# Kernel optimization log

Hardware: AMD Instinct MI355X
Metric: run time of the kernel (lower is better)

Reference implementation:

```python
import jax, jax.numpy as jnp
import numpy as np

N, D, E = 40000, 128, 640000
SLOPE = 0.01  # torch LeakyReLU default negative_slope

def leaky(x):
    return jnp.where(x >= 0, x, SLOPE * x)

def setup_inputs() -> dict:
    key = jax.random.key(0)
    ks = jax.random.split(key, 12)
    s = lambda fan_in: 1.0 / np.sqrt(fan_in)
    inp = {
        "x": jax.random.normal(ks[0], (N, D), jnp.float32),
        "pos": jax.random.normal(ks[1], (N, 3), jnp.float32),
        "edge_index": jax.random.randint(ks[2], (2, E), 0, N, jnp.int64),
        # mlp_h: Linear(D,D) -> LeakyReLU -> Linear(D,3) -> Tanh
        "Wh1": jax.random.uniform(ks[3], (D, D), jnp.float32, -s(D), s(D)),
        "bh1": jnp.zeros((D,), jnp.float32),
        "Wh2": jax.random.uniform(ks[4], (D, 3), jnp.float32, -s(D), s(D)),
        "bh2": jnp.zeros((3,), jnp.float32),
        # mlp_f: Linear(D+3, D) -> LeakyReLU
        "Wf1": jax.random.uniform(ks[5], (D + 3, D), jnp.float32, -s(D + 3), s(D + 3)),
        "bf1": jnp.zeros((D,), jnp.float32),
        # mlp_g: Linear(D,D) -> LeakyReLU -> Linear(D,D)
        "Wg1": jax.random.uniform(ks[6], (D, D), jnp.float32, -s(D), s(D)),
        "bg1": jnp.zeros((D,), jnp.float32),
        "Wg2": jax.random.uniform(ks[7], (D, D), jnp.float32, -s(D), s(D)),
        "bg2": jnp.zeros((D,), jnp.float32),
    }
    return inp

def reference(x, pos, edge_index, Wh1, bh1, Wh2, bh2, Wf1, bf1, Wg1, bg1, Wg2, bg2):
    src = edge_index[0]  # j (source / neighbor)
    dst = edge_index[1]  # i (target / center)
    n = x.shape[0]
    # mlp_h per node: predicted position offset delta_i
    delta = jnp.tanh(leaky(x @ Wh1 + bh1) @ Wh2 + bh2)  # [N, 3]
    # per-edge message: mlp_f(cat(pos_j - pos_i + delta_i, x_j))
    rel = pos[src] - pos[dst] + delta[dst]               # [E, 3]
    e = jnp.concatenate([rel, x[src]], axis=-1)          # [E, D+3]
    msg = leaky(e @ Wf1 + bf1)                           # [E, D]
    # sum aggregation to target nodes
    aggr = jax.ops.segment_sum(msg, dst, num_segments=n) # [N, D]
    # node update with residual
    out = x + (leaky(aggr @ Wg1 + bg1) @ Wg2 + bg2)      # [N, D]
    return out
```

## Files before the change

### kernel.cpp

```cpp
#include <hip/hip_runtime.h>

#define NN 40000
#define DD 128
#define EE 640000
#define SLOPE 0.01f
#define CAP 64

typedef __attribute__((ext_vector_type(8))) short  short8;
typedef __attribute__((ext_vector_type(8))) unsigned short ushort8;
typedef __attribute__((ext_vector_type(4))) float  floatx4;

__device__ __forceinline__ float leaky1(float v) { return v >= 0.f ? v : v * SLOPE; }

__device__ __forceinline__ unsigned short f2bf(float f) {
    unsigned int u = __float_as_uint(f);
    u += 0x7fffu + ((u >> 16) & 1u);
    return (unsigned short)(u >> 16);
}

__global__ __launch_bounds__(256) void k_init(
    const float* __restrict__ Wh1, const float* __restrict__ Wf1,
    const float* __restrict__ Wg1, const float* __restrict__ Wg2,
    int* __restrict__ cnt, unsigned short* __restrict__ pk)
{
    const int gid = blockIdx.x * 256 + threadIdx.x;
    if (gid < NN) cnt[gid] = 0;

    if (gid < 8192) {
        const int mat = gid >> 11;
        const int rem = gid & 2047;
        const int ct  = rem >> 8;
        const int kc  = (rem >> 6) & 3;
        const int l   = rem & 63;
        const float* W = (mat == 0) ? Wh1 : (mat == 1) ? (Wf1 + 3 * DD)
                       : (mat == 2) ? Wg1 : Wg2;
        const int n  = ct * 16 + (l & 15);
        const int k0 = kc * 32 + (l >> 4) * 8;
        ushort8 v;
        #pragma unroll
        for (int j = 0; j < 8; ++j) v[j] = f2bf(W[(size_t)(k0 + j) * DD + n]);
        *(ushort8*)(pk + (size_t)gid * 8) = v;
    }
}

__global__ __launch_bounds__(256) void k_node_pre(
    const float* __restrict__ x,
    const unsigned short* __restrict__ pk,
    const float* __restrict__ pos, const float* __restrict__ Wf1,
    const float* __restrict__ bh1, const float* __restrict__ Wh2,
    const float* __restrict__ bh2, const float* __restrict__ bf1,
    unsigned short* __restrict__ ub, float* __restrict__ delta)
{
    __shared__ unsigned short ul[64 * 136];
    const int t  = threadIdx.x;
    const int w  = t >> 6, l = t & 63;
    const int lm = l & 15, q = l >> 4;
    const bool upath = blockIdx.x < 625;
    const int tile = upath ? blockIdx.x : blockIdx.x - 625;
    const int rowb = tile * 64;
    const int row0 = rowb + w * 16;

    const unsigned short* pkm = upath ? (pk + 16384) : pk;

    floatx4 acc[8];
    #pragma unroll
    for (int ct = 0; ct < 8; ++ct) acc[ct] = 0.f;

    #pragma unroll
    for (int kc = 0; kc < 4; ++kc) {
        const float* xp = x + (size_t)(row0 + lm) * DD + kc * 32 + q * 8;
        const float4 v0 = *(const float4*)(xp);
        const float4 v1 = *(const float4*)(xp + 4);
        ushort8 au;
        au[0] = f2bf(v0.x); au[1] = f2bf(v0.y); au[2] = f2bf(v0.z); au[3] = f2bf(v0.w);
        au[4] = f2bf(v1.x); au[5] = f2bf(v1.y); au[6] = f2bf(v1.z); au[7] = f2bf(v1.w);
        const short8 a = *(short8*)&au;
        #pragma unroll
        for (int ct = 0; ct < 8; ++ct) {
            const short8 b = *(const short8*)(pkm + (size_t)((ct * 4 + kc) * 64 + l) * 8);
            acc[ct] = __builtin_amdgcn_mfma_f32_16x16x32_bf16(a, b, acc[ct], 0, 0, 0);
        }
    }

    if (upath) {
        float px[4][3];
        #pragma unroll
        for (int r = 0; r < 4; ++r) {
            const int rr = row0 + q * 4 + r;
            px[r][0] = pos[rr * 3 + 0];
            px[r][1] = pos[rr * 3 + 1];
            px[r][2] = pos[rr * 3 + 2];
        }
        #pragma unroll
        for (int ct = 0; ct < 8; ++ct) {
            const int col = ct * 16 + lm;
            const float bfv = bf1[col];
            const float w0 = Wf1[0 * DD + col];
            const float w1 = Wf1[1 * DD + col];
            const float w2 = Wf1[2 * DD + col];
            #pragma unroll
            for (int r = 0; r < 4; ++r) {
                const float uv = acc[ct][r] + bfv
                               + px[r][0] * w0 + px[r][1] * w1 + px[r][2] * w2;
                ul[(w * 16 + q * 4 + r) * 136 + col] = f2bf(uv);
            }
        }
        __syncthreads();
        #pragma unroll
        for (int k = 0; k < 4; ++k) {
            const int idx = t + k * 256;
            const int row = idx >> 4;
            const int c8  = (idx & 15) * 8;
            *(ushort8*)(ub + (size_t)(rowb + row) * DD + c8) =
                *(const ushort8*)(ul + row * 136 + c8);
        }
    } else {
        float p[4][3] = {};
        #pragma unroll
        for (int ct = 0; ct < 8; ++ct) {
            const int col = ct * 16 + lm;
            const float b1 = bh1[col];
            const float wh20 = Wh2[col * 3 + 0];
            const float wh21 = Wh2[col * 3 + 1];
            const float wh22 = Wh2[col * 3 + 2];
            #pragma unroll
            for (int r = 0; r < 4; ++r) {
                const float hv = leaky1(acc[ct][r] + b1);
                p[r][0] += hv * wh20;
                p[r][1] += hv * wh21;
                p[r][2] += hv * wh22;
            }
        }
        #pragma unroll
        for (int m = 1; m < 16; m <<= 1) {
            #pragma unroll
            for (int r = 0; r < 4; ++r) {
                #pragma unroll
                for (int k = 0; k < 3; ++k)
                    p[r][k] += __shfl_xor(p[r][k], m);
            }
        }
        if (lm < 12) {
            const int r = lm / 3, k = lm - 3 * (lm / 3);
            delta[(size_t)(row0 + q * 4 + r) * 3 + k] = tanhf(p[r][k] + bh2[k]);
        }
    }
}

__global__ __launch_bounds__(256) void k_scatter(const int* __restrict__ ei,
                                                 int* __restrict__ cnt,
                                                 int* __restrict__ esrc)
{
    const int g   = blockIdx.x & 7;
    const int lb  = blockIdx.x >> 3;
    const int dlo = g * 5000;
    const int dhi = dlo + 5000;

    for (int e = lb * 256 + threadIdx.x; e < EE; e += 65536) {
        const int dst = ei[EE + e];
        if (dst >= dlo && dst < dhi) {
            const int src = ei[e];
            const int p = atomicAdd(&cnt[dst], 1);
            if (p < CAP) esrc[(size_t)dst * CAP + p] = src;
        }
    }
}

__global__ __launch_bounds__(256) void k_gather(
    const int* __restrict__ cnt, const int* __restrict__ esrc,
    const float* __restrict__ pos, const float* __restrict__ delta,
    const float* __restrict__ Wf1, const unsigned short* __restrict__ ub,
    unsigned short* __restrict__ aggrb)
{
    const int t    = threadIdx.x;
    const int lane = t & 63;
    const int n    = blockIdx.x * 4 + (t >> 6);
    const int c2   = lane * 2;

    const float2 w0 = *(const float2*)(Wf1 + 0 * DD + c2);
    const float2 w1 = *(const float2*)(Wf1 + 1 * DD + c2);
    const float2 w2 = *(const float2*)(Wf1 + 2 * DD + c2);

    const float q0 = delta[n * 3 + 0] - pos[n * 3 + 0];
    const float q1 = delta[n * 3 + 1] - pos[n * 3 + 1];
    const float q2 = delta[n * 3 + 2] - pos[n * 3 + 2];

    const float v0 = q0 * w0.x + q1 * w1.x + q2 * w2.x;
    const float v1 = q0 * w0.y + q1 * w1.y + q2 * w2.y;

    const int s_all = esrc[(size_t)n * CAP + lane];
    const int d = min(cnt[n], CAP);

    float a0 = 0.f, a1 = 0.f, b0 = 0.f, b1 = 0.f;

    for (int j = 0; j < d; j += 8) {
        unsigned int u[8];
        bool vld[8];
        #pragma unroll
        for (int k = 0; k < 8; ++k) {
            const int jj = j + k;
            vld[k] = jj < d;
            int src = __shfl(s_all, jj & 63);
            src = vld[k] ? src : 0;
            u[k] = *(const unsigned int*)(ub + (size_t)src * DD + c2);
        }
        #pragma unroll
        for (int k = 0; k < 8; ++k) {
            const float e0 = __uint_as_float(u[k] << 16) + v0;
            const float e1 = __uint_as_float(u[k] & 0xffff0000u) + v1;
            const float r0 = vld[k] ? leaky1(e0) : 0.f;
            const float r1 = vld[k] ? leaky1(e1) : 0.f;
            if (k & 1) { b0 += r0; b1 += r1; }
            else       { a0 += r0; a1 += r1; }
        }
    }

    a0 += b0; a1 += b1;
    const unsigned int st = ((unsigned int)f2bf(a1) << 16) | (unsigned int)f2bf(a0);
    *(unsigned int*)(aggrb + (size_t)n * DD + c2) = st;
}

__global__ __launch_bounds__(256) void k_node_out(
    const unsigned short* __restrict__ aggrb, const unsigned short* __restrict__ pk,
    const float* __restrict__ x,
    const float* __restrict__ bg1, const float* __restrict__ bg2,
    float* __restrict__ out)
{
    __shared__ unsigned short gl[64 * 136];
    __shared__ float          ol[64 * 132];
    const int t  = threadIdx.x;
    const int w  = t >> 6, l = t & 63;
    const int lm = l & 15, q = l >> 4;
    const int rowb = blockIdx.x * 64;
    const int row0 = rowb + w * 16;

    const unsigned short* pkg1 = pk + 32768;
    const unsigned short* pkg2 = pk + 49152;

    floatx4 gacc[8];
    #pragma unroll
    for (int ct = 0; ct < 8; ++ct) gacc[ct] = 0.f;

    #pragma unroll
    for (int kc = 0; kc < 4; ++kc) {
        const short8 a = *(const short8*)(aggrb + (size_t)(row0 + lm) * DD + kc * 32 + q * 8);
        #pragma unroll
        for (int ct = 0; ct < 8; ++ct) {
            const short8 b = *(const short8*)(pkg1 + (size_t)((ct * 4 + kc) * 64 + l) * 8);
            gacc[ct] = __builtin_amdgcn_mfma_f32_16x16x32_bf16(a, b, gacc[ct], 0, 0, 0);
        }
    }

    #pragma unroll
    for (int ct = 0; ct < 8; ++ct) {
        const int col = ct * 16 + lm;
        const float b1 = bg1[col];
        #pragma unroll
        for (int r = 0; r < 4; ++r)
            gl[(w * 16 + q * 4 + r) * 136 + col] = f2bf(leaky1(gacc[ct][r] + b1));
    }
    __syncthreads();

    floatx4 oacc[8];
    #pragma unroll
    for (int ct = 0; ct < 8; ++ct) oacc[ct] = 0.f;

    #pragma unroll
    for (int kc = 0; kc < 4; ++kc) {
        const short8 a = *(const short8*)(gl + (size_t)(w * 16 + lm) * 136 + kc * 32 + q * 8);
        #pragma unroll
        for (int ct = 0; ct < 8; ++ct) {
            const short8 b = *(const short8*)(pkg2 + (size_t)((ct * 4 + kc) * 64 + l) * 8);
            oacc[ct] = __builtin_amdgcn_mfma_f32_16x16x32_bf16(a, b, oacc[ct], 0, 0, 0);
        }
    }

    __syncthreads();
    #pragma unroll
    for (int ct = 0; ct < 8; ++ct) {
        const int col = ct * 16 + lm;
        #pragma unroll
        for (int r = 0; r < 4; ++r)
            ol[(w * 16 + q * 4 + r) * 132 + col] = oacc[ct][r];
    }
    __syncthreads();

    #pragma unroll
    for (int k = 0; k < 8; ++k) {
        const int idx = t + k * 256;
        const int row = idx >> 5;
        const int c4  = (idx & 31) * 4;
        const float4 ov = *(const float4*)(ol + row * 132 + c4);
        const float4 bv = *(const float4*)(bg2 + c4);
        const size_t o  = (size_t)(rowb + row) * DD + c4;
        const float4 xv = *(const float4*)(x + o);
        float4 rv;
        rv.x = xv.x + ov.x + bv.x;
        rv.y = xv.y + ov.y + bv.y;
        rv.z = xv.z + ov.z + bv.z;
        rv.w = xv.w + ov.w + bv.w;
        *(float4*)(out + o) = rv;
    }
}

extern "C" void kernel_launch(void* const* d_in, const int* in_sizes, int n_in,
                              void* d_out, int out_size, void* d_ws, size_t ws_size,
                              hipStream_t stream)
{
    const float* x   = (const float*)d_in[0];
    const float* pos = (const float*)d_in[1];
    const int*   ei  = (const int*)d_in[2];
    const float* Wh1 = (const float*)d_in[3];
    const float* bh1 = (const float*)d_in[4];
    const float* Wh2 = (const float*)d_in[5];
    const float* bh2 = (const float*)d_in[6];
    const float* Wf1 = (const float*)d_in[7];
    const float* bf1 = (const float*)d_in[8];
    const float* Wg1 = (const float*)d_in[9];
    const float* bg1 = (const float*)d_in[10];
    const float* Wg2 = (const float*)d_in[11];
    const float* bg2 = (const float*)d_in[12];
    float* out = (float*)d_out;

    unsigned short* ub    = (unsigned short*)d_ws;
    unsigned short* aggrb = ub + (size_t)NN * DD;
    unsigned short* pk    = aggrb + (size_t)NN * DD;
    float* delta = (float*)(pk + 65536);
    int*   cnt   = (int*)(delta + (size_t)NN * 3);
    int*   esrc  = cnt + NN;

    k_init<<<160, 256, 0, stream>>>(Wh1, Wf1, Wg1, Wg2, cnt, pk);
    k_node_pre<<<1250, 256, 0, stream>>>(x, pk, pos, Wf1, bh1, Wh2, bh2, bf1,
                                         ub, delta);
    k_scatter<<<2048, 256, 0, stream>>>(ei, cnt, esrc);
    k_gather<<<NN / 4, 256, 0, stream>>>(cnt, esrc, pos, delta, Wf1, ub, aggrb);
    k_node_out<<<NN / 64, 256, 0, stream>>>(aggrb, pk, x, bg1, bg2, out);
}
```

Before: 183.6 us.

## Share x tile across both node MLP paths and store edge sources as 16-bit

k_node_pre now launches 512-thread blocks in which the first four waves compute the Wf1 projection and the last four compute the mlp_h delta. Both groups read one bf16 copy of the x tile that is converted once and staged in shared memory, so x is loaded and converted once per row instead of twice. Separately, the CSR-like edge source buffer is stored as unsigned short instead of int, halving its write and read traffic in scatter and gather. Node indices go up to 40000, which fits in 16 bits. The larger block and extra shared memory may lower occupancy.

```diff
diff --git a/kernel.cpp b/kernel.cpp
--- a/kernel.cpp
+++ b/kernel.cpp
@@ -43,7 +43,7 @@
     }
 }
 
-__global__ __launch_bounds__(256) void k_node_pre(
+__global__ __launch_bounds__(512) void k_node_pre(
     const float* __restrict__ x,
     const unsigned short* __restrict__ pk,
     const float* __restrict__ pos, const float* __restrict__ Wf1,
@@ -51,15 +51,32 @@
     const float* __restrict__ bh2, const float* __restrict__ bf1,
     unsigned short* __restrict__ ub, float* __restrict__ delta)
 {
+    __shared__ unsigned short xt[64 * 136];
     __shared__ unsigned short ul[64 * 136];
     const int t  = threadIdx.x;
     const int w  = t >> 6, l = t & 63;
     const int lm = l & 15, q = l >> 4;
-    const bool upath = blockIdx.x < 625;
-    const int tile = upath ? blockIdx.x : blockIdx.x - 625;
-    const int rowb = tile * 64;
-    const int row0 = rowb + w * 16;
-
+    const int rowb = blockIdx.x * 64;
+
+    {
+        const int row = t >> 3;
+        const int c0  = (t & 7) * 16;
+        const float* xp = x + (size_t)(rowb + row) * DD + c0;
+        #pragma unroll
+        for (int p = 0; p < 2; ++p) {
+            const float4 v0 = *(const float4*)(xp + p * 8);
+            const float4 v1 = *(const float4*)(xp + p * 8 + 4);
+            ushort8 o;
+            o[0] = f2bf(v0.x); o[1] = f2bf(v0.y); o[2] = f2bf(v0.z); o[3] = f2bf(v0.w);
+            o[4] = f2bf(v1.x); o[5] = f2bf(v1.y); o[6] = f2bf(v1.z); o[7] = f2bf(v1.w);
+            *(ushort8*)(xt + row * 136 + c0 + p * 8) = o;
+        }
+    }
+    __syncthreads();
+
+    const bool upath = w < 4;
+    const int wl   = upath ? w : w - 4;
+    const int row0 = wl * 16;
     const unsigned short* pkm = upath ? (pk + 16384) : pk;
 
     floatx4 acc[8];
@@ -68,13 +85,7 @@
 
     #pragma unroll
     for (int kc = 0; kc < 4; ++kc) {
-        const float* xp = x + (size_t)(row0 + lm) * DD + kc * 32 + q * 8;
-        const float4 v0 = *(const float4*)(xp);
-        const float4 v1 = *(const float4*)(xp + 4);
-        ushort8 au;
-        au[0] = f2bf(v0.x); au[1] = f2bf(v0.y); au[2] = f2bf(v0.z); au[3] = f2bf(v0.w);
-        au[4] = f2bf(v1.x); au[5] = f2bf(v1.y); au[6] = f2bf(v1.z); au[7] = f2bf(v1.w);
-        const short8 a = *(short8*)&au;
+        const short8 a = *(const short8*)(xt + (row0 + lm) * 136 + kc * 32 + q * 8);
         #pragma unroll
         for (int ct = 0; ct < 8; ++ct) {
             const short8 b = *(const short8*)(pkm + (size_t)((ct * 4 + kc) * 64 + l) * 8);
@@ -86,7 +97,7 @@
         float px[4][3];
         #pragma unroll
         for (int r = 0; r < 4; ++r) {
-            const int rr = row0 + q * 4 + r;
+            const int rr = rowb + row0 + q * 4 + r;
             px[r][0] = pos[rr * 3 + 0];
             px[r][1] = pos[rr * 3 + 1];
             px[r][2] = pos[rr * 3 + 2];
@@ -102,17 +113,8 @@
             for (int r = 0; r < 4; ++r) {
                 const float uv = acc[ct][r] + bfv
                                + px[r][0] * w0 + px[r][1] * w1 + px[r][2] * w2;
-                ul[(w * 16 + q * 4 + r) * 136 + col] = f2bf(uv);
+                ul[(row0 + q * 4 + r) * 136 + col] = f2bf(uv);
             }
-        }
-        __syncthreads();
-        #pragma unroll
-        for (int k = 0; k < 4; ++k) {
-            const int idx = t + k * 256;
-            const int row = idx >> 4;
-            const int c8  = (idx & 15) * 8;
-            *(ushort8*)(ub + (size_t)(rowb + row) * DD + c8) =
-                *(const ushort8*)(ul + row * 136 + c8);
         }
     } else {
         float p[4][3] = {};
@@ -142,14 +144,24 @@
         }
         if (lm < 12) {
             const int r = lm / 3, k = lm - 3 * (lm / 3);
-            delta[(size_t)(row0 + q * 4 + r) * 3 + k] = tanhf(p[r][k] + bh2[k]);
-        }
+            delta[(size_t)(rowb + row0 + q * 4 + r) * 3 + k] = tanhf(p[r][k] + bh2[k]);
+        }
+    }
+    __syncthreads();
+
+    #pragma unroll
+    for (int k = 0; k < 2; ++k) {
+        const int idx = t + k * 512;
+        const int row = idx >> 4;
+        const int c8  = (idx & 15) * 8;
+        *(ushort8*)(ub + (size_t)(rowb + row) * DD + c8) =
+            *(const ushort8*)(ul + row * 136 + c8);
     }
 }
 
 __global__ __launch_bounds__(256) void k_scatter(const int* __restrict__ ei,
                                                  int* __restrict__ cnt,
-                                                 int* __restrict__ esrc)
+                                                 unsigned short* __restrict__ esrc)
 {
     const int g   = blockIdx.x & 7;
     const int lb  = blockIdx.x >> 3;
@@ -161,13 +173,13 @@
         if (dst >= dlo && dst < dhi) {
             const int src = ei[e];
             const int p = atomicAdd(&cnt[dst], 1);
-            if (p < CAP) esrc[(size_t)dst * CAP + p] = src;
+            if (p < CAP) esrc[(size_t)dst * CAP + p] = (unsigned short)src;
         }
     }
 }
 
 __global__ __launch_bounds__(256) void k_gather(
-    const int* __restrict__ cnt, const int* __restrict__ esrc,
+    const int* __restrict__ cnt, const unsigned short* __restrict__ esrc,
     const float* __restrict__ pos, const float* __restrict__ delta,
     const float* __restrict__ Wf1, const unsigned short* __restrict__ ub,
     unsigned short* __restrict__ aggrb)
@@ -188,7 +200,7 @@
     const float v0 = q0 * w0.x + q1 * w1.x + q2 * w2.x;
     const float v1 = q0 * w0.y + q1 * w1.y + q2 * w2.y;
 
-    const int s_all = esrc[(size_t)n * CAP + lane];
+    const int s_all = (int)esrc[(size_t)n * CAP + lane];
     const int d = min(cnt[n], CAP);
 
     float a0 = 0.f, a1 = 0.f, b0 = 0.f, b1 = 0.f;
@@ -327,11 +339,11 @@
     unsigned short* pk    = aggrb + (size_t)NN * DD;
     float* delta = (float*)(pk + 65536);
     int*   cnt   = (int*)(delta + (size_t)NN * 3);
-    int*   esrc  = cnt + NN;
+    unsigned short* esrc = (unsigned short*)(cnt + NN);
 
     k_init<<<160, 256, 0, stream>>>(Wh1, Wf1, Wg1, Wg2, cnt, pk);
-    k_node_pre<<<1250, 256, 0, stream>>>(x, pk, pos, Wf1, bh1, Wh2, bh2, bf1,
-                                         ub, delta);
+    k_node_pre<<<625, 512, 0, stream>>>(x, pk, pos, Wf1, bh1, Wh2, bh2, bf1,
+                                        ub, delta);
     k_scatter<<<2048, 256, 0, stream>>>(ei, cnt, esrc);
     k_gather<<<NN / 4, 256, 0, stream>>>(cnt, esrc, pos, delta, Wf1, ub, aggrb);
     k_node_out<<<NN / 64, 256, 0, stream>>>(aggrb, pk, x, bg1, bg2, out);
```

Result: no change. 182.3 us (-0.7%).
